# Performance work log

Measured on AMD Instinct MI355X. Metric: run time of the kernel, lower is better.

The kernel has to match this reference:

```python
import jax, jax.numpy as jnp
import numpy as np

N = 250000          # number of points (also used as padded #unique voxels)
EPS = 1e-5          # BatchNorm1d eps
DIMS = [9, 64, 128, 256, 64]
PROJ = 16


def _bn(x, g, b):
    # torch BatchNorm1d in training mode: biased batch var
    m = jnp.mean(x, axis=0)
    v = jnp.var(x, axis=0)
    return (x - m) * jax.lax.rsqrt(v + EPS) * g + b


def setup_inputs() -> dict:
    key = jax.random.key(0)
    ks = list(jax.random.split(key, 24))
    inp = {
        "feats": jax.random.normal(ks[0], (N, DIMS[0]), jnp.float32),
        "coords": jax.random.randint(ks[1], (N, 3), 0, 48, jnp.int32),
    }
    k = 2
    # 4 BatchNorms over dims 9, 64, 128, 256
    for i, d in enumerate(DIMS[:4]):
        inp[f"bn{i}_g"] = jnp.ones((d,), jnp.float32)
        inp[f"bn{i}_b"] = jnp.zeros((d,), jnp.float32)
    # 4 Linear layers 9->64->128->256->64, stored as [in, out]
    for i in range(4):
        fin, fout = DIMS[i], DIMS[i + 1]
        inp[f"w{i+1}"] = jax.random.normal(ks[k], (fin, fout), jnp.float32) * (1.0 / np.sqrt(fin)); k += 1
        inp[f"b{i+1}"] = jnp.zeros((fout,), jnp.float32)
    # feature projection 64 -> 16 (kaiming-ish init, bias 0.01)
    inp["wp"] = jax.random.normal(ks[k], (DIMS[4], PROJ), jnp.float32) * np.sqrt(2.0 / PROJ); k += 1
    inp["bp"] = jnp.full((PROJ,), 0.01, jnp.float32)
    return inp


def reference(feats, coords, bn0_g, bn0_b, bn1_g, bn1_b, bn2_g, bn2_b, bn3_g, bn3_b,
              w1, b1, w2, b2, w3, b3, w4, b4, wp, bp):
    # unique voxel coords (sorted rows, like torch.unique dim=0); padded to N for jit
    unq, inv, cnt = jnp.unique(coords, axis=0, return_inverse=True, return_counts=True,
                               size=N, fill_value=-1)
    inv = inv.reshape(-1)

    # point MLP: BN -> Lin -> BN -> ReLU -> Lin -> BN -> ReLU -> Lin -> BN -> ReLU -> Lin
    x = _bn(feats, bn0_g, bn0_b)
    x = jax.nn.relu(_bn(x @ w1 + b1, bn1_g, bn1_b))
    x = jax.nn.relu(_bn(x @ w2 + b2, bn2_g, bn2_b))
    x = jax.nn.relu(_bn(x @ w3 + b3, bn3_g, bn3_b))
    x = x @ w4 + b4                                   # [N, 64]

    # scatter_max pooling per voxel; empty (padding) segments zeroed
    pooled = jax.ops.segment_max(x, inv, num_segments=N)
    pooled = jnp.where((cnt > 0)[:, None], pooled, 0.0)

    # feature projection + ReLU
    pooled = jax.nn.relu(pooled @ wp + bp)            # [N, 16] (rows >= #unique are padding)
    return pooled, unq.astype(jnp.int32)
```

## Files before the change

### kernel.cpp

```cpp
#include <hip/hip_runtime.h>
#include <hip/hip_bf16.h>

#define EPSBN 1e-5f
#define NKEYS 110592
#define SLICES 64
#define VPW 8

typedef __attribute__((ext_vector_type(8))) short bf16x8;
typedef __attribute__((ext_vector_type(4))) float f32x4;

__device__ __forceinline__ float bf2f(ushort u){ return __uint_as_float(((unsigned)u)<<16); }
__device__ __forceinline__ ushort f2bf(float f){
  unsigned u = __float_as_uint(f);
  unsigned r = u + 0x7fffu + ((u>>16)&1u);
  return (ushort)(r>>16);
}

template<int KP>
__device__ __forceinline__ int swz(int row, int kbyte){
  constexpr int MASK = (KP >= 64) ? 7 : 3;
  return row*(KP*2) + (kbyte ^ ((row & MASK) << 4));
}

__device__ __forceinline__ int tri(int k, int l){
  if (k > l){ int t=k; k=l; l=t; }
  return k*9 - (k*(k-1))/2 + (l-k);
}

__global__ __launch_bounds__(256) void k_zero(uint4* __restrict__ p, size_t n16){
  size_t i = (size_t)blockIdx.x*256 + threadIdx.x;
  size_t stride = (size_t)gridDim.x*256;
  uint4 z = make_uint4(0,0,0,0);
  for (; i < n16; i += stride) p[i] = z;
}

__global__ __launch_bounds__(256) void k_wprep(const float* __restrict__ w,
    ushort* __restrict__ wf, int K, int M){
  int CT = M >> 4;
  int KS = (K + 31) >> 5;
  int total = KS*CT*512;
  for (int idx = blockIdx.x*256 + threadIdx.x; idx < total; idx += gridDim.x*256){
    int e = idx & 7, l = (idx>>3) & 63, c = idx >> 9;
    int ct = c % CT, ks = c / CT;
    int g = l >> 4, j = l & 15;
    int k = ks*32 + g*8 + e, col = ct*16 + j;
    wf[idx] = (k < K) ? f2bf(w[(size_t)k*M + col]) : (ushort)0;
  }
}

__global__ __launch_bounds__(256) void k_keys(const int* __restrict__ coords,
    unsigned* __restrict__ cnt, int n){
  int i = blockIdx.x*256 + threadIdx.x;
  if (i >= n) return;
  int x = coords[3*i+0], y = coords[3*i+1], z = coords[3*i+2];
  atomicAdd(&cnt[(unsigned)((x*48 + y)*48 + z)], 1u);
}

__global__ __launch_bounds__(256) void k_scan1(const unsigned* __restrict__ cnt,
    unsigned* __restrict__ rloc, unsigned* __restrict__ ploc, unsigned* __restrict__ bsum){
  __shared__ unsigned tf[256], tc[256];
  int t = threadIdx.x;
  int base = blockIdx.x*1024 + t*4;
  uint4 cv = *(const uint4*)&cnt[base];
  unsigned f0 = cv.x?1u:0u, f1 = cv.y?1u:0u, f2 = cv.z?1u:0u, f3 = cv.w?1u:0u;
  unsigned sf = f0+f1+f2+f3;
  unsigned sc = cv.x+cv.y+cv.z+cv.w;
  tf[t] = sf; tc[t] = sc;
  __syncthreads();
  for (int off=1; off<256; off<<=1){
    unsigned af = (t>=off) ? tf[t-off] : 0u;
    unsigned ac = (t>=off) ? tc[t-off] : 0u;
    __syncthreads();
    tf[t] += af; tc[t] += ac;
    __syncthreads();
  }
  unsigned rf = tf[t] - sf, rc = tc[t] - sc;
  rloc[base+0] = rf; rf += f0;    ploc[base+0] = rc; rc += cv.x;
  rloc[base+1] = rf; rf += f1;    ploc[base+1] = rc; rc += cv.y;
  rloc[base+2] = rf; rf += f2;    ploc[base+2] = rc; rc += cv.z;
  rloc[base+3] = rf;              ploc[base+3] = rc;
  if (t == 255){ bsum[2*blockIdx.x] = tf[255]; bsum[2*blockIdx.x+1] = tc[255]; }
}

__global__ __launch_bounds__(128) void k_scan2(const unsigned* __restrict__ bsum,
    unsigned* __restrict__ boff){
  __shared__ unsigned tf[128], tc[128];
  int t = threadIdx.x;
  unsigned vf = (t < 108) ? bsum[2*t] : 0u;
  unsigned vc = (t < 108) ? bsum[2*t+1] : 0u;
  tf[t] = vf; tc[t] = vc;
  __syncthreads();
  for (int off=1; off<128; off<<=1){
    unsigned af = (t>=off) ? tf[t-off] : 0u;
    unsigned ac = (t>=off) ? tc[t-off] : 0u;
    __syncthreads();
    tf[t] += af; tc[t] += ac;
    __syncthreads();
  }
  boff[2*t] = tf[t] - vf;
  boff[2*t+1] = tc[t] - vc;
}

__global__ __launch_bounds__(256) void k_unq(const unsigned* __restrict__ cnt,
    const unsigned* __restrict__ rloc, const unsigned* __restrict__ ploc,
    const unsigned* __restrict__ boff, float* __restrict__ unq,
    unsigned* __restrict__ vst, unsigned* __restrict__ vct){
  int k = blockIdx.x*256 + threadIdx.x;
  if (k >= NKEYS) return;
  unsigned c = cnt[k];
  if (c == 0) return;
  unsigned r  = rloc[k] + boff[2*(k>>10)];
  unsigned st = ploc[k] + boff[2*(k>>10)+1];
  float z = (float)(k % 48);
  float y = (float)((k/48) % 48);
  float x = (float)(k / 2304);
  unq[3*(size_t)r+0] = x; unq[3*(size_t)r+1] = y; unq[3*(size_t)r+2] = z;
  vst[r] = st; vct[r] = c;
}

__global__ __launch_bounds__(256) void k_csr(const int* __restrict__ coords,
    const unsigned* __restrict__ ploc, const unsigned* __restrict__ boff,
    unsigned* __restrict__ cursor, unsigned* __restrict__ csr, int n){
  int i = blockIdx.x*256 + threadIdx.x;
  if (i >= n) return;
  int x = coords[3*i+0], y = coords[3*i+1], z = coords[3*i+2];
  unsigned k = (unsigned)((x*48 + y)*48 + z);
  unsigned slot = atomicAdd(&cursor[k], 1u);
  unsigned st = ploc[k] + boff[2*(k>>10)+1];
  csr[st + slot] = i;
}

__global__ __launch_bounds__(256) void k_stats0x(const float* __restrict__ X,
    float* __restrict__ slices, int n){
  float s[9], q[45];
  #pragma unroll
  for (int k=0;k<9;k++) s[k]=0.f;
  #pragma unroll
  for (int i=0;i<45;i++) q[i]=0.f;
  int stride = gridDim.x*256;
  for (int i = blockIdx.x*256 + threadIdx.x; i < n; i += stride){
    float v[9];
    #pragma unroll
    for (int k=0;k<9;k++) v[k] = X[(size_t)i*9+k];
    int qi=0;
    #pragma unroll
    for (int k=0;k<9;k++){
      s[k] += v[k];
      #pragma unroll
      for (int l=k;l<9;l++) q[qi++] += v[k]*v[l];
    }
  }
  #pragma unroll
  for (int off=32; off>0; off>>=1){
    #pragma unroll
    for (int k=0;k<9;k++)  s[k] += __shfl_down(s[k], off, 64);
    #pragma unroll
    for (int i=0;i<45;i++) q[i] += __shfl_down(q[i], off, 64);
  }
  if ((threadIdx.x & 63) == 0){
    float* sl = slices + (size_t)(blockIdx.x & (SLICES-1))*54;
    #pragma unroll
    for (int k=0;k<9;k++)  atomicAdd(&sl[k],   s[k]);
    #pragma unroll
    for (int i=0;i<45;i++) atomicAdd(&sl[9+i], q[i]);
  }
}

__global__ __launch_bounds__(256) void k_fin01(const float* __restrict__ slices, float invN,
    const float* __restrict__ g0, const float* __restrict__ b0,
    const float* __restrict__ g1, const float* __restrict__ b1,
    const float* __restrict__ w1, float* __restrict__ ac0, float* __restrict__ ac1){
  __shared__ float pa[4][64];
  __shared__ float red[54];
  __shared__ float ms[9], a0s[9], c0s[9];
  int t = threadIdx.x;
  {
    int col = t & 63, ch = t >> 6;
    float a = 0.f;
    if (col < 54){
      #pragma unroll 4
      for (int sl = ch*16; sl < ch*16 + 16; sl++) a += slices[(size_t)sl*54 + col];
    }
    pa[ch][col] = a;
  }
  __syncthreads();
  if (t < 54) red[t] = pa[0][t] + pa[1][t] + pa[2][t] + pa[3][t];
  __syncthreads();
  if (t < 9){
    float m = red[t]*invN;
    float var = red[9 + tri(t,t)]*invN - m*m;
    float a0 = g0[t]*rsqrtf(var + EPSBN);
    float c0 = b0[t] - m*a0;
    ms[t] = m; a0s[t] = a0; c0s[t] = c0;
    ac0[t] = a0; ac0[9+t] = c0;
  }
  __syncthreads();
  if (t < 64){
    float wj[9];
    #pragma unroll
    for (int k=0;k<9;k++) wj[k] = w1[(size_t)k*64 + t];
    float mean = 0.f;
    #pragma unroll
    for (int k=0;k<9;k++) mean += (ms[k]*a0s[k] + c0s[k])*wj[k];
    float e2 = 0.f;
    #pragma unroll
    for (int k=0;k<9;k++)
      #pragma unroll
      for (int l=0;l<9;l++){
        float U = a0s[k]*a0s[l]*(red[9 + tri(k,l)]*invN)
                + a0s[k]*c0s[l]*ms[k] + a0s[l]*c0s[k]*ms[l] + c0s[k]*c0s[l];
        e2 += wj[k]*wj[l]*U;
      }
    float var = e2 - mean*mean;
    float a = g1[t]*rsqrtf(var + EPSBN);
    ac1[t] = a;
    ac1[64+t] = b1[t] - mean*a;
  }
}

__global__ __launch_bounds__(256) void k_fin(const float* __restrict__ slices, int M, float invN,
    const float* __restrict__ g, const float* __restrict__ b, float* __restrict__ ac){
  __shared__ float ps[4][64], pss[4][64];
  int t = threadIdx.x;
  int col = t & 63, ch = t >> 6;
  int j = blockIdx.x*64 + col;
  float s = 0.f, ss = 0.f;
  #pragma unroll 4
  for (int sl = ch*16; sl < ch*16 + 16; sl++){
    s  += slices[(size_t)sl*2*M + j];
    ss += slices[(size_t)sl*2*M + M + j];
  }
  ps[ch][col] = s; pss[ch][col] = ss;
  __syncthreads();
  if (t < 64){
    j = blockIdx.x*64 + t;
    float S  = ps[0][t]+ps[1][t]+ps[2][t]+ps[3][t];
    float SS = pss[0][t]+pss[1][t]+pss[2][t]+pss[3][t];
    float mean = S*invN;
    float var = SS*invN - mean*mean;
    float a = g[j]*rsqrtf(var + EPSBN);
    ac[j] = a;
    ac[M+j] = b[j] - mean*a;
  }
}

template<int DEPTH>
__global__ __launch_bounds__(256,2) void k_chain(
    const float* __restrict__ feats, const float* __restrict__ ac0,
    const ushort* __restrict__ w1f, const float* __restrict__ ac1,
    const ushort* __restrict__ w2f, const float* __restrict__ ac2,
    const ushort* __restrict__ w3f, const float* __restrict__ ac3,
    const ushort* __restrict__ w4f, const float* __restrict__ b4,
    const unsigned* __restrict__ csr, ushort* __restrict__ y4,
    float* __restrict__ slices, int n){
  constexpr int SMEM = (DEPTH==2) ? 12288 : (DEPTH==3) ? 28672 : 32768;
  __shared__ __align__(16) char smem[SMEM];
  __shared__ unsigned rid_s[64];
  char* X0 = smem;

  int t = threadIdx.x;
  int lane = t & 63, w = t >> 6;
  int lrow = lane & 15, lgrp = lane >> 4;
  int rowbase = blockIdx.x * 64;

  bf16x8 b1 = *(const bf16x8*)(w1f + (size_t)(w*64 + lane)*8);

  if constexpr (DEPTH == 4){
    if (t < 64){
      int gr = rowbase + t;
      rid_s[t] = (gr < n) ? csr[gr] : 0u;
    }
    __syncthreads();
  }

  for (int e = t; e < 2048; e += 256){
    int row = e >> 5, k = e & 31;
    int gr = rowbase + row;
    size_t rid = (DEPTH == 4) ? (size_t)rid_s[row] : (size_t)gr;
    float v = (k < 9 && gr < n) ? fmaf(feats[rid*9 + k], ac0[k], ac0[9+k]) : 0.f;
    *(ushort*)(X0 + swz<32>(row, k*2)) = f2bf(v);
  }
  __syncthreads();

  f32x4 acc0[4] = {};
  #pragma unroll
  for (int rb = 0; rb < 4; rb++){
    bf16x8 a = *(const bf16x8*)(X0 + swz<32>(rb*16 + lrow, lgrp*16));
    acc0[rb] = __builtin_amdgcn_mfma_f32_16x16x32_bf16(a, b1, acc0[rb], 0,0,0);
  }

  char* T1 = smem + 4096;
  {
    int j = w*16 + lrow;
    float a1 = ac1[j], c1 = ac1[64+j];
    #pragma unroll
    for (int rb=0;rb<4;rb++)
      #pragma unroll
      for (int r=0;r<4;r++){
        int row = rb*16 + 4*lgrp + r;
        float v = fmaxf(fmaf(acc0[rb][r], a1, c1), 0.f);
        if (rowbase + row >= n) v = 0.f;
        *(ushort*)(T1 + swz<64>(row, j*2)) = f2bf(v);
      }
  }
  __syncthreads();

  f32x4 acc1[4][2] = {};
  #pragma unroll
  for (int ks=0; ks<2; ks++){
    bf16x8 bb[2];
    #pragma unroll
    for (int f=0;f<2;f++)
      bb[f] = *(const bf16x8*)(w2f + (size_t)((ks*8 + 2*w + f)*64 + lane)*8);
    #pragma unroll
    for (int rb=0;rb<4;rb++){
      bf16x8 a = *(const bf16x8*)(T1 + swz<64>(rb*16 + lrow, ks*64 + lgrp*16));
      #pragma unroll
      for (int f=0;f<2;f++)
        acc1[rb][f] = __builtin_amdgcn_mfma_f32_16x16x32_bf16(a, bb[f], acc1[rb][f], 0,0,0);
    }
  }

  if constexpr (DEPTH == 2){
    float s[2]={0.f,0.f}, ss[2]={0.f,0.f};
    #pragma unroll
    for (int rb=0;rb<4;rb++)
      #pragma unroll
      for (int f=0;f<2;f++)
        #pragma unroll
        for (int r=0;r<4;r++){ float v=acc1[rb][f][r]; s[f]+=v; ss[f]+=v*v; }
    __syncthreads();
    float* ssum = (float*)smem;
    ssum[t] = 0.f;
    __syncthreads();
    #pragma unroll
    for (int f=0;f<2;f++){
      int j = w*32 + 16*f + lrow;
      atomicAdd(&ssum[j], s[f]); atomicAdd(&ssum[128+j], ss[f]);
    }
    __syncthreads();
    float* gsl = slices + (size_t)(blockIdx.x & (SLICES-1))*256;
    atomicAdd(&gsl[t], ssum[t]);
    return;
  }

  if constexpr (DEPTH >= 3){
  char* T2 = smem + 12288;
  #pragma unroll
  for (int f=0;f<2;f++){
    int j = w*32 + 16*f + lrow;
    float a2 = ac2[j], c2 = ac2[128+j];
    #pragma unroll
    for (int rb=0;rb<4;rb++)
      #pragma unroll
      for (int r=0;r<4;r++){
        int row = rb*16 + 4*lgrp + r;
        float v = fmaxf(fmaf(acc1[rb][f][r], a2, c2), 0.f);
        if (rowbase + row >= n) v = 0.f;
        *(ushort*)(T2 + swz<128>(row, j*2)) = f2bf(v);
      }
  }
  __syncthreads();

  if constexpr (DEPTH == 3){
    float s3[2][2], ss3[2][2];
    #pragma unroll
    for (int h=0; h<2; h++){
      f32x4 acc2[4][2] = {};
      #pragma unroll
      for (int ks=0; ks<4; ks++){
        bf16x8 bb[2];
        #pragma unroll
        for (int f=0;f<2;f++)
          bb[f] = *(const bf16x8*)(w3f + (size_t)((ks*16 + 4*w + 2*h + f)*64 + lane)*8);
        #pragma unroll
        for (int rb=0;rb<4;rb++){
          bf16x8 a = *(const bf16x8*)(T2 + swz<128>(rb*16 + lrow, ks*64 + lgrp*16));
          #pragma unroll
          for (int f=0;f<2;f++)
            acc2[rb][f] = __builtin_amdgcn_mfma_f32_16x16x32_bf16(a, bb[f], acc2[rb][f], 0,0,0);
        }
      }
      #pragma unroll
      for (int f=0;f<2;f++){
        float s=0.f, ss=0.f;
        #pragma unroll
        for (int rb=0;rb<4;rb++)
          #pragma unroll
          for (int r=0;r<4;r++){ float v=acc2[rb][f][r]; s+=v; ss+=v*v; }
        s3[h][f]=s; ss3[h][f]=ss;
      }
    }
    __syncthreads();
    float* ssum = (float*)smem;
    for (int e=t; e<512; e+=256) ssum[e] = 0.f;
    __syncthreads();
    #pragma unroll
    for (int h=0;h<2;h++)
      #pragma unroll
      for (int f=0;f<2;f++){
        int j = 64*w + 32*h + 16*f + lrow;
        atomicAdd(&ssum[j], s3[h][f]); atomicAdd(&ssum[256+j], ss3[h][f]);
      }
    __syncthreads();
    float* gsl = slices + (size_t)(blockIdx.x & (SLICES-1))*512;
    for (int e=t; e<512; e+=256) atomicAdd(&gsl[e], ssum[e]);
    return;
  }

  if constexpr (DEPTH == 4){
  f32x4 acc2[4][4] = {};
  #pragma unroll
  for (int ks=0; ks<4; ks++){
    bf16x8 bb[4];
    #pragma unroll
    for (int f=0;f<4;f++)
      bb[f] = *(const bf16x8*)(w3f + (size_t)((ks*16 + 4*w + f)*64 + lane)*8);
    #pragma unroll
    for (int rb=0;rb<4;rb++){
      bf16x8 a = *(const bf16x8*)(T2 + swz<128>(rb*16 + lrow, ks*64 + lgrp*16));
      #pragma unroll
      for (int f=0;f<4;f++)
        acc2[rb][f] = __builtin_amdgcn_mfma_f32_16x16x32_bf16(a, bb[f], acc2[rb][f], 0,0,0);
    }
  }
  __syncthreads();

  char* X3 = smem;
  #pragma unroll
  for (int f=0;f<4;f++){
    int j = 64*w + 16*f + lrow;
    float a3 = ac3[j], c3 = ac3[256+j];
    #pragma unroll
    for (int rb=0;rb<4;rb++)
      #pragma unroll
      for (int r=0;r<4;r++){
        int row = rb*16 + 4*lgrp + r;
        float v = fmaxf(fmaf(acc2[rb][f][r], a3, c3), 0.f);
        if (rowbase + row >= n) v = 0.f;
        *(ushort*)(X3 + swz<256>(row, j*2)) = f2bf(v);
      }
  }
  __syncthreads();

  f32x4 acc3[4] = {};
  #pragma unroll
  for (int ks=0; ks<8; ks++){
    bf16x8 b = *(const bf16x8*)(w4f + (size_t)((ks*4 + w)*64 + lane)*8);
    #pragma unroll
    for (int rb=0;rb<4;rb++){
      bf16x8 a = *(const bf16x8*)(X3 + swz<256>(rb*16 + lrow, ks*64 + lgrp*16));
      acc3[rb] = __builtin_amdgcn_mfma_f32_16x16x32_bf16(a, b, acc3[rb], 0,0,0);
    }
  }

  {
    int j = w*16 + lrow;
    float bias4 = b4[j];
    #pragma unroll
    for (int rb=0;rb<4;rb++)
      #pragma unroll
      for (int r=0;r<4;r++){
        int gr = rowbase + 16*rb + 4*lgrp + r;
        if (gr < n) y4[(size_t)gr*64 + j] = f2bf(acc3[rb][r] + bias4);
      }
  }
  }
  }
}

__global__ __launch_bounds__(256) void k_pool(const ushort* __restrict__ y4,
    const unsigned* __restrict__ vst, const unsigned* __restrict__ vct,
    const unsigned* __restrict__ boff, const float* __restrict__ wp,
    const float* __restrict__ bp, float* __restrict__ out, int n){
  __shared__ float wpsT[1024];
  __shared__ float sm[4][64];
  int t = threadIdx.x, w = t >> 6, lane = t & 63;
  for (int e=t; e<1024; e+=256){
    int j = e >> 6, ch = e & 63;
    wpsT[e] = wp[ch*16 + j];
  }
  __syncthreads();
  unsigned M = boff[216];
  int base = blockIdx.x*(4*VPW) + w*VPW;
  if (base >= (int)M) return;
  float bpv = (lane < 16) ? bp[lane] : 0.f;
  int q = lane >> 4, j = lane & 15;
  int vend = (int)M - base; if (vend > VPW) vend = VPW;
  for (int v = 0; v < vend; v++){
    int r = base + v;
    unsigned st = vst[r], c = vct[r];
    const ushort* row = y4 + (size_t)st*64 + lane;
    float m = bf2f(row[0]);
    #pragma unroll 4
    for (unsigned pp = 1; pp < c; pp++)
      m = fmaxf(m, bf2f(row[(size_t)pp*64]));
    sm[w][lane] = m;
    float acc = 0.f;
    #pragma unroll
    for (int i=0;i<16;i++) acc = fmaf(sm[w][q*16+i], wpsT[j*64 + q*16+i], acc);
    acc += __shfl_xor(acc, 16, 64);
    acc += __shfl_xor(acc, 32, 64);
    if (lane < 16) out[(size_t)r*16 + lane] = fmaxf(acc + bpv, 0.f);
  }
}

__global__ __launch_bounds__(256) void k_fill(const unsigned* __restrict__ boff,
    const float* __restrict__ bp, float* __restrict__ out,
    float* __restrict__ unq, int n){
  int r = blockIdx.x*256 + threadIdx.x;
  if (r >= n) return;
  unsigned M = boff[216];
  if ((unsigned)r < M) return;
  #pragma unroll
  for (int j=0;j<16;j++) out[(size_t)r*16 + j] = fmaxf(bp[j], 0.f);
  unq[3*(size_t)r+0] = -1.f; unq[3*(size_t)r+1] = -1.f; unq[3*(size_t)r+2] = -1.f;
}

extern "C" void kernel_launch(void* const* d_in, const int* in_sizes, int n_in,
                              void* d_out, int out_size, void* d_ws, size_t ws_size,
                              hipStream_t stream){
  (void)n_in; (void)out_size;
  const float* feats  = (const float*)d_in[0];
  const int*   coords = (const int*)d_in[1];
  const float* g0=(const float*)d_in[2];  const float* bb0=(const float*)d_in[3];
  const float* g1=(const float*)d_in[4];  const float* bb1=(const float*)d_in[5];
  const float* g2=(const float*)d_in[6];  const float* bb2=(const float*)d_in[7];
  const float* g3=(const float*)d_in[8];  const float* bb3=(const float*)d_in[9];
  const float* w1=(const float*)d_in[10];
  const float* w2=(const float*)d_in[12];
  const float* w3=(const float*)d_in[14];
  const float* w4=(const float*)d_in[16]; const float* b4=(const float*)d_in[17];
  const float* wp=(const float*)d_in[18]; const float* bp=(const float*)d_in[19];
  int n = in_sizes[0]/9;

  char* ws = (char*)d_ws;
  size_t off = 0;
  auto alloc = [&](size_t bytes){ size_t o = off; off = (off + bytes + 255) & ~(size_t)255; return o; };
  size_t o_cnt  = alloc((size_t)NKEYS*4);
  size_t o_cur  = alloc((size_t)NKEYS*4);
  size_t o_sl0  = alloc((size_t)SLICES*54*4);
  size_t o_sl2  = alloc((size_t)SLICES*256*4);
  size_t o_sl3  = alloc((size_t)SLICES*512*4);
  size_t zero_end = off;
  size_t o_rloc = alloc((size_t)NKEYS*4);
  size_t o_ploc = alloc((size_t)NKEYS*4);
  size_t o_bsum = alloc(256*4);
  size_t o_boff = alloc(256*4);
  size_t o_ac0  = alloc(18*4);
  size_t o_ac1  = alloc(128*4);
  size_t o_ac2  = alloc(256*4);
  size_t o_ac3  = alloc(512*4);
  size_t o_w1f  = alloc(2048*2);
  size_t o_w2f  = alloc(8192*2);
  size_t o_w3f  = alloc(32768*2);
  size_t o_w4f  = alloc(16384*2);
  size_t o_csr  = alloc((size_t)n*4);
  size_t o_vst  = alloc((size_t)n*4);
  size_t o_vct  = alloc((size_t)n*4);
  size_t o_y4   = alloc((size_t)n*64*2);
  if (ws_size < off) return;

  unsigned* cnt  = (unsigned*)(ws + o_cnt);
  unsigned* cursor = (unsigned*)(ws + o_cur);
  unsigned* rloc = (unsigned*)(ws + o_rloc);
  unsigned* ploc = (unsigned*)(ws + o_ploc);
  unsigned* bsum = (unsigned*)(ws + o_bsum);
  unsigned* boff = (unsigned*)(ws + o_boff);
  float* sl0 = (float*)(ws + o_sl0);
  float* sl2 = (float*)(ws + o_sl2);
  float* sl3 = (float*)(ws + o_sl3);
  float* ac0 = (float*)(ws + o_ac0);
  float* ac1 = (float*)(ws + o_ac1);
  float* ac2 = (float*)(ws + o_ac2);
  float* ac3 = (float*)(ws + o_ac3);
  ushort* w1f = (ushort*)(ws + o_w1f);
  ushort* w2f = (ushort*)(ws + o_w2f);
  ushort* w3f = (ushort*)(ws + o_w3f);
  ushort* w4f = (ushort*)(ws + o_w4f);
  unsigned* csr = (unsigned*)(ws + o_csr);
  unsigned* vst = (unsigned*)(ws + o_vst);
  unsigned* vct = (unsigned*)(ws + o_vct);
  ushort* y4 = (ushort*)(ws + o_y4);

  float* out_pool = (float*)d_out;
  float* out_unq  = out_pool + (size_t)n*16;

  {
    size_t n16 = zero_end/16;
    int zb = (int)((n16 + 255)/256); if (zb > 2048) zb = 2048;
    k_zero<<<zb,256,0,stream>>>((uint4*)ws, n16);
  }

  k_wprep<<<8,256,0,stream>>>(w1, w1f, 9, 64);
  k_wprep<<<32,256,0,stream>>>(w2, w2f, 64, 128);
  k_wprep<<<128,256,0,stream>>>(w3, w3f, 128, 256);
  k_wprep<<<64,256,0,stream>>>(w4, w4f, 256, 64);

  int nb = (n + 255)/256;
  k_keys<<<nb,256,0,stream>>>(coords, cnt, n);
  k_scan1<<<NKEYS/1024,256,0,stream>>>(cnt, rloc, ploc, bsum);
  k_scan2<<<1,128,0,stream>>>(bsum, boff);
  k_unq<<<(NKEYS+255)/256,256,0,stream>>>(cnt, rloc, ploc, boff, out_unq, vst, vct);
  k_csr<<<nb,256,0,stream>>>(coords, ploc, boff, cursor, csr, n);

  k_stats0x<<<512,256,0,stream>>>(feats, sl0, n);
  k_fin01<<<1,256,0,stream>>>(sl0, 1.f/(float)n, g0, bb0, g1, bb1, w1, ac0, ac1);

  int gb = (n+63)/64;
  k_chain<2><<<gb,256,0,stream>>>(feats, ac0, w1f, ac1, w2f, ac2, w3f, ac3, w4f, b4, nullptr, nullptr, sl2, n);
  k_fin<<<2,256,0,stream>>>(sl2, 128, 1.f/(float)n, g2, bb2, ac2);

  k_chain<3><<<gb,256,0,stream>>>(feats, ac0, w1f, ac1, w2f, ac2, w3f, ac3, w4f, b4, nullptr, nullptr, sl3, n);
  k_fin<<<4,256,0,stream>>>(sl3, 256, 1.f/(float)n, g3, bb3, ac3);

  k_chain<4><<<gb,256,0,stream>>>(feats, ac0, w1f, ac1, w2f, ac2, w3f, ac3, w4f, b4, csr, y4, nullptr, n);

  int maxv = (n < NKEYS) ? n : NKEYS;
  k_pool<<<(maxv + 4*VPW - 1)/(4*VPW),256,0,stream>>>(y4, vst, vct, boff, wp, bp, out_pool, n);
  k_fill<<<nb,256,0,stream>>>(boff, bp, out_pool, out_unq, n);
}
```

Measured before the change: 301.6 us.

## Materialize layer-2 pre-BN activations to skip recomputing early MLP layers

```diff
diff --git a/kernel.cpp b/kernel.cpp
--- a/kernel.cpp
+++ b/kernel.cpp
@@ -244,6 +244,238 @@
   }
 }
 
+__global__ __launch_bounds__(256,2) void k_chain12(
+    const float* __restrict__ feats, const float* __restrict__ ac0,
+    const ushort* __restrict__ w1f, const float* __restrict__ ac1,
+    const ushort* __restrict__ w2f, const unsigned* __restrict__ csr,
+    ushort* __restrict__ t2, float* __restrict__ slices, int n){
+  __shared__ __align__(16) char smem[12288];
+  __shared__ unsigned rid_s[64];
+  char* X0 = smem;
+  char* T1 = smem + 4096;
+  int t = threadIdx.x;
+  int lane = t & 63, w = t >> 6;
+  int lrow = lane & 15, lgrp = lane >> 4;
+  int rowbase = blockIdx.x * 64;
+
+  bf16x8 b1 = *(const bf16x8*)(w1f + (size_t)(w*64 + lane)*8);
+  if (t < 64){
+    int gr = rowbase + t;
+    rid_s[t] = (gr < n) ? csr[gr] : 0u;
+  }
+  __syncthreads();
+  for (int e = t; e < 2048; e += 256){
+    int row = e >> 5, k = e & 31;
+    int gr = rowbase + row;
+    float v = (k < 9 && gr < n) ? fmaf(feats[(size_t)rid_s[row]*9 + k], ac0[k], ac0[9+k]) : 0.f;
+    *(ushort*)(X0 + swz<32>(row, k*2)) = f2bf(v);
+  }
+  __syncthreads();
+
+  f32x4 acc0[4] = {};
+  #pragma unroll
+  for (int rb = 0; rb < 4; rb++){
+    bf16x8 a = *(const bf16x8*)(X0 + swz<32>(rb*16 + lrow, lgrp*16));
+    acc0[rb] = __builtin_amdgcn_mfma_f32_16x16x32_bf16(a, b1, acc0[rb], 0,0,0);
+  }
+  {
+    int j = w*16 + lrow;
+    float a1 = ac1[j], c1 = ac1[64+j];
+    #pragma unroll
+    for (int rb=0;rb<4;rb++)
+      #pragma unroll
+      for (int r=0;r<4;r++){
+        int row = rb*16 + 4*lgrp + r;
+        float v = fmaxf(fmaf(acc0[rb][r], a1, c1), 0.f);
+        if (rowbase + row >= n) v = 0.f;
+        *(ushort*)(T1 + swz<64>(row, j*2)) = f2bf(v);
+      }
+  }
+  __syncthreads();
+
+  f32x4 acc1[4][2] = {};
+  #pragma unroll
+  for (int ks=0; ks<2; ks++){
+    bf16x8 bb[2];
+    #pragma unroll
+    for (int f=0;f<2;f++)
+      bb[f] = *(const bf16x8*)(w2f + (size_t)((ks*8 + 2*w + f)*64 + lane)*8);
+    #pragma unroll
+    for (int rb=0;rb<4;rb++){
+      bf16x8 a = *(const bf16x8*)(T1 + swz<64>(rb*16 + lrow, ks*64 + lgrp*16));
+      #pragma unroll
+      for (int f=0;f<2;f++)
+        acc1[rb][f] = __builtin_amdgcn_mfma_f32_16x16x32_bf16(a, bb[f], acc1[rb][f], 0,0,0);
+    }
+  }
+
+  float s[2]={0.f,0.f}, ss[2]={0.f,0.f};
+  #pragma unroll
+  for (int rb=0;rb<4;rb++)
+    #pragma unroll
+    for (int f=0;f<2;f++)
+      #pragma unroll
+      for (int r=0;r<4;r++){
+        int gr = rowbase + rb*16 + 4*lgrp + r;
+        if (gr < n){
+          ushort h = f2bf(acc1[rb][f][r]);
+          t2[(size_t)gr*128 + w*32 + 16*f + lrow] = h;
+          float fr = bf2f(h);
+          s[f] += fr; ss[f] += fr*fr;
+        }
+      }
+  __syncthreads();
+  float* ssum = (float*)smem;
+  ssum[t] = 0.f;
+  __syncthreads();
+  #pragma unroll
+  for (int f=0;f<2;f++){
+    int j = w*32 + 16*f + lrow;
+    atomicAdd(&ssum[j], s[f]); atomicAdd(&ssum[128+j], ss[f]);
+  }
+  __syncthreads();
+  float* gsl = slices + (size_t)(blockIdx.x & (SLICES-1))*256;
+  atomicAdd(&gsl[t], ssum[t]);
+}
+
+__device__ __forceinline__ void stage_T2(char* T2, const ushort* __restrict__ t2,
+    const float* __restrict__ ac2, int rowbase, int t, int n){
+  for (int e = t; e < 1024; e += 256){
+    int row = e >> 4, k8 = (e & 15) << 3;
+    int gr = rowbase + row;
+    bf16x8 v = {};
+    if (gr < n) v = *(const bf16x8*)(t2 + (size_t)gr*128 + k8);
+    float4 A0 = *(const float4*)(ac2 + k8),       A1 = *(const float4*)(ac2 + k8 + 4);
+    float4 C0 = *(const float4*)(ac2 + 128 + k8), C1 = *(const float4*)(ac2 + 128 + k8 + 4);
+    float Av[8] = {A0.x,A0.y,A0.z,A0.w,A1.x,A1.y,A1.z,A1.w};
+    float Cv[8] = {C0.x,C0.y,C0.z,C0.w,C1.x,C1.y,C1.z,C1.w};
+    bf16x8 o;
+    #pragma unroll
+    for (int i=0;i<8;i++){
+      float f = (gr < n) ? fmaxf(fmaf(bf2f((ushort)v[i]), Av[i], Cv[i]), 0.f) : 0.f;
+      o[i] = f2bf(f);
+    }
+    *(bf16x8*)(T2 + swz<128>(row, k8*2)) = o;
+  }
+}
+
+__global__ __launch_bounds__(256,2) void k_stage3(
+    const ushort* __restrict__ t2, const float* __restrict__ ac2,
+    const ushort* __restrict__ w3f, float* __restrict__ slices, int n){
+  __shared__ __align__(16) char smem[16384];
+  char* T2 = smem;
+  int t = threadIdx.x;
+  int lane = t & 63, w = t >> 6;
+  int lrow = lane & 15, lgrp = lane >> 4;
+  int rowbase = blockIdx.x * 64;
+  stage_T2(T2, t2, ac2, rowbase, t, n);
+  __syncthreads();
+
+  f32x4 acc2[4][4] = {};
+  #pragma unroll
+  for (int ks=0; ks<4; ks++){
+    bf16x8 bb[4];
+    #pragma unroll
+    for (int f=0;f<4;f++)
+      bb[f] = *(const bf16x8*)(w3f + (size_t)((ks*16 + 4*w + f)*64 + lane)*8);
+    #pragma unroll
+    for (int rb=0;rb<4;rb++){
+      bf16x8 a = *(const bf16x8*)(T2 + swz<128>(rb*16 + lrow, ks*64 + lgrp*16));
+      #pragma unroll
+      for (int f=0;f<4;f++)
+        acc2[rb][f] = __builtin_amdgcn_mfma_f32_16x16x32_bf16(a, bb[f], acc2[rb][f], 0,0,0);
+    }
+  }
+  __syncthreads();
+  float* ssum = (float*)smem;
+  for (int e=t; e<512; e+=256) ssum[e] = 0.f;
+  __syncthreads();
+  #pragma unroll
+  for (int f=0;f<4;f++){
+    float s=0.f, ss=0.f;
+    #pragma unroll
+    for (int rb=0;rb<4;rb++)
+      #pragma unroll
+      for (int r=0;r<4;r++){ float v=acc2[rb][f][r]; s+=v; ss+=v*v; }
+    int j = 64*w + 16*f + lrow;
+    atomicAdd(&ssum[j], s); atomicAdd(&ssum[256+j], ss);
+  }
+  __syncthreads();
+  float* gsl = slices + (size_t)(blockIdx.x & (SLICES-1))*512;
+  for (int e=t; e<512; e+=256) atomicAdd(&gsl[e], ssum[e]);
+}
+
+__global__ __launch_bounds__(256,2) void k_stage34(
+    const ushort* __restrict__ t2, const float* __restrict__ ac2,
+    const ushort* __restrict__ w3f, const float* __restrict__ ac3,
+    const ushort* __restrict__ w4f, const float* __restrict__ b4,
+    ushort* __restrict__ y4, int n){
+  __shared__ __align__(16) char smem[32768];
+  char* T2 = smem + 16384;
+  char* X3 = smem;
+  int t = threadIdx.x;
+  int lane = t & 63, w = t >> 6;
+  int lrow = lane & 15, lgrp = lane >> 4;
+  int rowbase = blockIdx.x * 64;
+  stage_T2(T2, t2, ac2, rowbase, t, n);
+  __syncthreads();
+
+  f32x4 acc2[4][4] = {};
+  #pragma unroll
+  for (int ks=0; ks<4; ks++){
+    bf16x8 bb[4];
+    #pragma unroll
+    for (int f=0;f<4;f++)
+      bb[f] = *(const bf16x8*)(w3f + (size_t)((ks*16 + 4*w + f)*64 + lane)*8);
+    #pragma unroll
+    for (int rb=0;rb<4;rb++){
+      bf16x8 a = *(const bf16x8*)(T2 + swz<128>(rb*16 + lrow, ks*64 + lgrp*16));
+      #pragma unroll
+      for (int f=0;f<4;f++)
+        acc2[rb][f] = __builtin_amdgcn_mfma_f32_16x16x32_bf16(a, bb[f], acc2[rb][f], 0,0,0);
+    }
+  }
+  __syncthreads();
+
+  #pragma unroll
+  for (int f=0;f<4;f++){
+    int j = 64*w + 16*f + lrow;
+    float a3 = ac3[j], c3 = ac3[256+j];
+    #pragma unroll
+    for (int rb=0;rb<4;rb++)
+      #pragma unroll
+      for (int r=0;r<4;r++){
+        int row = rb*16 + 4*lgrp + r;
+        float v = fmaxf(fmaf(acc2[rb][f][r], a3, c3), 0.f);
+        if (rowbase + row >= n) v = 0.f;
+        *(ushort*)(X3 + swz<256>(row, j*2)) = f2bf(v);
+      }
+  }
+  __syncthreads();
+
+  f32x4 acc3[4] = {};
+  #pragma unroll
+  for (int ks=0; ks<8; ks++){
+    bf16x8 b = *(const bf16x8*)(w4f + (size_t)((ks*4 + w)*64 + lane)*8);
+    #pragma unroll
+    for (int rb=0;rb<4;rb++){
+      bf16x8 a = *(const bf16x8*)(X3 + swz<256>(rb*16 + lrow, ks*64 + lgrp*16));
+      acc3[rb] = __builtin_amdgcn_mfma_f32_16x16x32_bf16(a, b, acc3[rb], 0,0,0);
+    }
+  }
+  {
+    int j = w*16 + lrow;
+    float bias4 = b4[j];
+    #pragma unroll
+    for (int rb=0;rb<4;rb++)
+      #pragma unroll
+      for (int r=0;r<4;r++){
+        int gr = rowbase + 16*rb + 4*lgrp + r;
+        if (gr < n) y4[(size_t)gr*64 + j] = f2bf(acc3[rb][r] + bias4);
+      }
+  }
+}
+
 template<int DEPTH>
 __global__ __launch_bounds__(256,2) void k_chain(
     const float* __restrict__ feats, const float* __restrict__ ac0,
@@ -257,14 +489,11 @@
   __shared__ __align__(16) char smem[SMEM];
   __shared__ unsigned rid_s[64];
   char* X0 = smem;
-
   int t = threadIdx.x;
   int lane = t & 63, w = t >> 6;
   int lrow = lane & 15, lgrp = lane >> 4;
   int rowbase = blockIdx.x * 64;
-
   bf16x8 b1 = *(const bf16x8*)(w1f + (size_t)(w*64 + lane)*8);
-
   if constexpr (DEPTH == 4){
     if (t < 64){
       int gr = rowbase + t;
@@ -272,7 +501,6 @@
     }
     __syncthreads();
   }
-
   for (int e = t; e < 2048; e += 256){
     int row = e >> 5, k = e & 31;
     int gr = rowbase + row;
@@ -281,14 +509,12 @@
     *(ushort*)(X0 + swz<32>(row, k*2)) = f2bf(v);
   }
   __syncthreads();
-
   f32x4 acc0[4] = {};
   #pragma unroll
   for (int rb = 0; rb < 4; rb++){
     bf16x8 a = *(const bf16x8*)(X0 + swz<32>(rb*16 + lrow, lgrp*16));
     acc0[rb] = __builtin_amdgcn_mfma_f32_16x16x32_bf16(a, b1, acc0[rb], 0,0,0);
   }
-
   char* T1 = smem + 4096;
   {
     int j = w*16 + lrow;
@@ -304,7 +530,6 @@
       }
   }
   __syncthreads();
-
   f32x4 acc1[4][2] = {};
   #pragma unroll
   for (int ks=0; ks<2; ks++){
@@ -320,7 +545,6 @@
         acc1[rb][f] = __builtin_amdgcn_mfma_f32_16x16x32_bf16(a, bb[f], acc1[rb][f], 0,0,0);
     }
   }
-
   if constexpr (DEPTH == 2){
     float s[2]={0.f,0.f}, ss[2]={0.f,0.f};
     #pragma unroll
@@ -343,7 +567,6 @@
     atomicAdd(&gsl[t], ssum[t]);
     return;
   }
-
   if constexpr (DEPTH >= 3){
   char* T2 = smem + 12288;
   #pragma unroll
@@ -361,7 +584,6 @@
       }
   }
   __syncthreads();
-
   if constexpr (DEPTH == 3){
     float s3[2][2], ss3[2][2];
     #pragma unroll
@@ -407,7 +629,6 @@
     for (int e=t; e<512; e+=256) atomicAdd(&gsl[e], ssum[e]);
     return;
   }
-
   if constexpr (DEPTH == 4){
   f32x4 acc2[4][4] = {};
   #pragma unroll
@@ -425,7 +646,6 @@
     }
   }
   __syncthreads();
-
   char* X3 = smem;
   #pragma unroll
   for (int f=0;f<4;f++){
@@ -442,7 +662,6 @@
       }
   }
   __syncthreads();
-
   f32x4 acc3[4] = {};
   #pragma unroll
   for (int ks=0; ks<8; ks++){
@@ -453,7 +672,6 @@
       acc3[rb] = __builtin_amdgcn_mfma_f32_16x16x32_bf16(a, b, acc3[rb], 0,0,0);
     }
   }
-
   {
     int j = w*16 + lrow;
     float bias4 = b4[j];
@@ -462,7 +680,9 @@
       #pragma unroll
       for (int r=0;r<4;r++){
         int gr = rowbase + 16*rb + 4*lgrp + r;
-        if (gr < n) y4[(size_t)gr*64 + j] = f2bf(acc3[rb][r] + bias4);
+        if (gr < n){
+          y4[(size_t)gr*64 + j] = f2bf(acc3[rb][r] + bias4);
+        }
       }
   }
   }
@@ -559,7 +779,11 @@
   size_t o_vst  = alloc((size_t)n*4);
   size_t o_vct  = alloc((size_t)n*4);
   size_t o_y4   = alloc((size_t)n*64*2);
-  if (ws_size < off) return;
+  size_t off_base = off;
+  size_t o_t2   = alloc((size_t)n*128*2);
+  size_t off_full = off;
+  if (ws_size < off_base) return;
+  bool bigws = (ws_size >= off_full);
 
   unsigned* cnt  = (unsigned*)(ws + o_cnt);
   unsigned* cursor = (unsigned*)(ws + o_cur);
@@ -582,6 +806,7 @@
   unsigned* vst = (unsigned*)(ws + o_vst);
   unsigned* vct = (unsigned*)(ws + o_vct);
   ushort* y4 = (ushort*)(ws + o_y4);
+  ushort* t2 = (ushort*)(ws + o_t2);
 
   float* out_pool = (float*)d_out;
   float* out_unq  = out_pool + (size_t)n*16;
@@ -608,13 +833,19 @@
   k_fin01<<<1,256,0,stream>>>(sl0, 1.f/(float)n, g0, bb0, g1, bb1, w1, ac0, ac1);
 
   int gb = (n+63)/64;
-  k_chain<2><<<gb,256,0,stream>>>(feats, ac0, w1f, ac1, w2f, ac2, w3f, ac3, w4f, b4, nullptr, nullptr, sl2, n);
-  k_fin<<<2,256,0,stream>>>(sl2, 128, 1.f/(float)n, g2, bb2, ac2);
-
-  k_chain<3><<<gb,256,0,stream>>>(feats, ac0, w1f, ac1, w2f, ac2, w3f, ac3, w4f, b4, nullptr, nullptr, sl3, n);
-  k_fin<<<4,256,0,stream>>>(sl3, 256, 1.f/(float)n, g3, bb3, ac3);
-
-  k_chain<4><<<gb,256,0,stream>>>(feats, ac0, w1f, ac1, w2f, ac2, w3f, ac3, w4f, b4, csr, y4, nullptr, n);
+  if (bigws){
+    k_chain12<<<gb,256,0,stream>>>(feats, ac0, w1f, ac1, w2f, csr, t2, sl2, n);
+    k_fin<<<2,256,0,stream>>>(sl2, 128, 1.f/(float)n, g2, bb2, ac2);
+    k_stage3<<<gb,256,0,stream>>>(t2, ac2, w3f, sl3, n);
+    k_fin<<<4,256,0,stream>>>(sl3, 256, 1.f/(float)n, g3, bb3, ac3);
+    k_stage34<<<gb,256,0,stream>>>(t2, ac2, w3f, ac3, w4f, b4, y4, n);
+  } else {
+    k_chain<2><<<gb,256,0,stream>>>(feats, ac0, w1f, ac1, w2f, ac2, w3f, ac3, w4f, b4, nullptr, nullptr, sl2, n);
+    k_fin<<<2,256,0,stream>>>(sl2, 128, 1.f/(float)n, g2, bb2, ac2);
+    k_chain<3><<<gb,256,0,stream>>>(feats, ac0, w1f, ac1, w2f, ac2, w3f, ac3, w4f, b4, nullptr, nullptr, sl3, n);
+    k_fin<<<4,256,0,stream>>>(sl3, 256, 1.f/(float)n, g3, bb3, ac3);
+    k_chain<4><<<gb,256,0,stream>>>(feats, ac0, w1f, ac1, w2f, ac2, w3f, ac3, w4f, b4, csr, y4, nullptr, n);
+  }
 
   int maxv = (n < NKEYS) ? n : NKEYS;
   k_pool<<<(maxv + 4*VPW - 1)/(4*VPW),256,0,stream>>>(y4, vst, vct, boff, wp, bp, out_pool, n);
```

Result: faster. 289.3 us (median of 4 runs) (-4.0%).
